# Performance work log

Measured on AMD Instinct MI355X. Metric: run time of the kernel, lower is better.

## Reference

```python
import jax, jax.numpy as jnp
import numpy as np

B, S, T = 32, 64, 64
E, H = 512, 512
V_SRC = 32000
V_TGT = 32000


def setup_inputs() -> dict:
    key = jax.random.key(0)
    ks = jax.random.split(key, 16)
    g = lambda i, shape: jax.random.normal(ks[i], shape, jnp.float32) * 0.05
    return {
        "src_sentences": jax.random.randint(ks[0], (B, S), 0, V_SRC),
        "target_sentences": jax.random.randint(ks[1], (B, T), 0, V_TGT),
        "source_sentence_length": jnp.full((B,), S, dtype=jnp.int32),
        "src_emb": g(2, (V_SRC, E)),
        "tgt_emb": g(3, (V_TGT, E)),
        "enc_Wih_f": g(4, (4 * H, E)), "enc_Whh_f": g(5, (4 * H, H)), "enc_b_f": jnp.zeros((4 * H,), jnp.float32),
        "enc_Wih_b": g(6, (4 * H, E)), "enc_Whh_b": g(7, (4 * H, H)), "enc_b_b": jnp.zeros((4 * H,), jnp.float32),
        "dec_Wih": g(8, (4 * H, E + H)), "dec_Whh": g(9, (4 * H, H)), "dec_b": jnp.zeros((4 * H,), jnp.float32),
        "W_att_src": g(10, (H, 2 * H)),
        "W_att_vec": g(11, (H, 3 * H)),
        "W_readout": g(12, (V_TGT, H)),
        "W_init": g(13, (H, 2 * H)), "b_init": jnp.zeros((H,), jnp.float32),
    }


def _lstm_cell(x, h, c, Wih, Whh, b):
    # PyTorch gate order: i, f, g, o ; b = b_ih + b_hh combined
    gates = x @ Wih.T + h @ Whh.T + b
    i, f, g, o = jnp.split(gates, 4, axis=-1)
    c_new = jax.nn.sigmoid(f) * c + jax.nn.sigmoid(i) * jnp.tanh(g)
    h_new = jax.nn.sigmoid(o) * jnp.tanh(c_new)
    return h_new, c_new


def _enc_dir(xs, lengths, Wih, Whh, b, reverse):
    # xs: [S, B, E]; emulates packed LSTM: state frozen / outputs zero at padded steps
    Sn, Bn, _ = xs.shape
    Hd = Whh.shape[1]
    ts = jnp.arange(Sn)

    def step(carry, inp):
        h, c = carry
        x, t = inp
        valid = (t < lengths)[:, None].astype(x.dtype)  # [B,1]
        h2, c2 = _lstm_cell(x, h, c, Wih, Whh, b)
        h = valid * h2 + (1.0 - valid) * h
        c = valid * c2 + (1.0 - valid) * c
        return (h, c), valid * h

    init = (jnp.zeros((Bn, Hd), xs.dtype), jnp.zeros((Bn, Hd), xs.dtype))
    (hT, cT), outs = jax.lax.scan(step, init, (xs, ts), reverse=reverse)
    return outs, hT, cT


def reference(src_sentences, target_sentences, source_sentence_length,
              src_emb, tgt_emb,
              enc_Wih_f, enc_Whh_f, enc_b_f,
              enc_Wih_b, enc_Whh_b, enc_b_b,
              dec_Wih, dec_Whh, dec_b,
              W_att_src, W_att_vec, W_readout, W_init, b_init):
    Bn, Sn = src_sentences.shape
    Hh = dec_Whh.shape[1]
    # faithful to original: embedding [B,S,E] then .view(S,B,E) (a reshape)
    src_x = src_emb[src_sentences].reshape(Sn, Bn, -1)  # [S,B,E]
    out_f, _, c_f = _enc_dir(src_x, source_sentence_length, enc_Wih_f, enc_Whh_f, enc_b_f, False)
    out_b, _, c_b = _enc_dir(src_x, source_sentence_length, enc_Wih_b, enc_Whh_b, enc_b_b, True)
    src_enc = jnp.concatenate([out_f, out_b], axis=-1).transpose(1, 0, 2)  # [B,S,2H]
    dec_c0 = jnp.concatenate([c_f, c_b], axis=-1) @ W_init.T + b_init
    dec_h0 = jnp.tanh(dec_c0)

    pad_mask = jnp.arange(Sn)[None, :] >= source_sentence_length[:, None]  # [B,S] True = pad
    src_att = src_enc @ W_att_src.T  # [B,S,H]
    ys = tgt_emb[target_sentences].transpose(1, 0, 2)  # [T,B,E]

    def dec_step(carry, y):
        h, c, att = carry
        x = jnp.concatenate([y, att], axis=-1)  # feed_input=True
        h, c = _lstm_cell(x, h, c, dec_Wih, dec_Whh, dec_b)
        score = jnp.einsum('bsh,bh->bs', src_att, h)
        score = jnp.where(pad_mask, -jnp.inf, score)
        alpha = jax.nn.softmax(score, axis=-1)
        ctx = jnp.einsum('bs,bsd->bd', alpha, src_enc)
        att = jnp.tanh(jnp.concatenate([h, ctx], axis=-1) @ W_att_vec.T)
        return (h, c, att), att

    att0 = jnp.zeros((Bn, Hh), src_x.dtype)
    _, att_ves = jax.lax.scan(dec_step, (dec_h0, dec_c0, att0), ys)  # [T,B,H]

    logp = jax.nn.log_softmax(att_ves @ W_readout.T, axis=-1)  # [T,B,V]
    logp = logp.transpose(1, 0, 2)  # [B,T,V]
    gold = jnp.take_along_axis(logp, target_sentences[:, :, None], axis=-1).squeeze(-1)  # [B,T]
    gold = gold * (target_sentences != 0).astype(logp.dtype)
    # faithful to original: permuted to batch-first then sum(dim=0) -> per-timestep sums, shape [T]
    return gold.sum(axis=0)
```

## Files before the change

kernel.cpp:

```cpp
#include <hip/hip_runtime.h>
#include <hip/hip_bf16.h>
#include <cmath>


__device__ __forceinline__ float sigf(float x){ return 1.0f/(1.0f+__expf(-x)); }

constexpr long o_senc   = 0;
constexpr long o_satt   = o_senc + 32L*64*1024;
constexpr long o_aves   = o_satt + 32L*64*512;
constexpr long o_hF     = o_aves + 64L*32*512;
constexpr long o_cF     = o_hF + 32L*512;
constexpr long o_hB     = o_cF + 32L*512;
constexpr long o_cB     = o_hB + 32L*512;
constexpr long o_sumexp = o_cB + 32L*512;
constexpr long o_gold   = o_sumexp + 2048;
constexpr long o_ccat   = o_gold + 2048;
constexpr long o_dech   = o_ccat + 32L*1024;
constexpr long o_decc   = o_dech + 32L*512;
constexpr long o_att    = o_decc + 32L*512;
constexpr long o_ctx    = o_att + 32L*512;
constexpr long o_gatesP = o_ctx + 32L*1024;
constexpr long o_attvP  = o_gatesP + 16L*65536;

__global__ void k_zero(float* p, int n){
    int i = blockIdx.x*256 + threadIdx.x;
    if (i < n) p[i] = 0.f;
}

__device__ __forceinline__ void gt_mac_store(const float (*Hs)[128], const float (*Ws)[129],
                                             float* __restrict__ P, int ldp, int n0){
    __syncthreads();
    int tid = threadIdx.x;
    int nl = tid & 63, bg = tid >> 6;
    float acc[8] = {};
    for (int k=0;k<128;++k){
        float w = Ws[nl][k];
        #pragma unroll
        for (int i=0;i<8;++i) acc[i] += Hs[bg*8+i][k] * w;
    }
    #pragma unroll
    for (int i=0;i<8;++i)
        P[(long)(bg*8+i)*ldp + n0 + nl] = acc[i];
}

__device__ __forceinline__ void gt_load_W(const float* __restrict__ W, int ldw, int kw, int n0,
                                          float (*Ws)[129]){
    int tid = threadIdx.x;
    int nl = tid >> 2, kl = (tid & 3) * 32;
    const float* wp = W + (long)(n0+nl)*ldw + kw + kl;
    #pragma unroll
    for (int i=0;i<32;i+=4){
        float4 v = *(const float4*)(wp + i);
        Ws[nl][kl+i+0]=v.x; Ws[nl][kl+i+1]=v.y; Ws[nl][kl+i+2]=v.z; Ws[nl][kl+i+3]=v.w;
    }
}

__device__ __forceinline__ void gates_tile_f32(
    const float* __restrict__ A, int lda, int k0,
    const float* __restrict__ W, int ldw, int kw, int n0,
    float* __restrict__ P, int ldp, float (*Hs)[128], float (*Ws)[129]){
    int tid = threadIdx.x;
    int bl = tid >> 3, kl = (tid & 7) * 16;
    const float* ap = A + (long)bl*lda + k0 + kl;
    float* hp = &Hs[bl][kl];
    #pragma unroll
    for (int i=0;i<16;i+=4){
        float4 v = *(const float4*)(ap + i);
        hp[i+0]=v.x; hp[i+1]=v.y; hp[i+2]=v.z; hp[i+3]=v.w;
    }
    gt_load_W(W, ldw, kw, n0, Ws);
    gt_mac_store(Hs, Ws, P, ldp, n0);
}

__device__ __forceinline__ void gates_tile_emb(
    const float* __restrict__ emb, const int* __restrict__ tok, int off, int stride, int k0,
    const float* __restrict__ W, int ldw, int kw, int n0,
    float* __restrict__ P, int ldp, float (*Hs)[128], float (*Ws)[129]){
    int tid = threadIdx.x;
    int bl = tid >> 3, kl = (tid & 7) * 16;
    const float* ap = emb + (long)tok[off + bl*stride]*512 + k0 + kl;
    float* hp = &Hs[bl][kl];
    #pragma unroll
    for (int i=0;i<16;i+=4){
        float4 v = *(const float4*)(ap + i);
        hp[i+0]=v.x; hp[i+1]=v.y; hp[i+2]=v.z; hp[i+3]=v.w;
    }
    gt_load_W(W, ldw, kw, n0, Ws);
    gt_mac_store(Hs, Ws, P, ldp, n0);
}

__global__ __launch_bounds__(256)
void k_enc_gates(const int* __restrict__ tok, const float* __restrict__ emb,
                 const float* __restrict__ hF, const float* __restrict__ hB,
                 const float* __restrict__ WihF, const float* __restrict__ WhhF,
                 const float* __restrict__ WihB, const float* __restrict__ WhhB,
                 float* __restrict__ gatesP, int s){
    __shared__ float Hs[32][128];
    __shared__ float Ws[64][129];
    int bx = blockIdx.x;
    int dir = bx >> 8, rem = bx & 255;
    int kc = rem & 7, nc = rem >> 3;
    int sd = dir ? 63 - s : s;
    float* P = gatesP + (long)(dir*8 + kc)*65536;
    if (kc < 4)
        gates_tile_emb(emb, tok, sd*32, 1, kc*128,
                       dir ? WihB : WihF, 512, kc*128, nc*64, P, 2048, Hs, Ws);
    else
        gates_tile_f32(dir ? hB : hF, 512, (kc-4)*128,
                       dir ? WhhB : WhhF, 512, (kc-4)*128, nc*64, P, 2048, Hs, Ws);
}

__global__ void k_enc_cell(const float* __restrict__ gatesP,
                           const float* __restrict__ bF, const float* __restrict__ bB,
                           float* hF, float* cF, float* hB, float* cB,
                           float* __restrict__ senc, const int* __restrict__ lens, int s){
    int idx = blockIdx.x*256 + threadIdx.x;
    int dir = idx >> 14, r = idx & 16383;
    int b = r >> 9, j = r & 511;
    int sd = dir ? (63 - s) : s;
    const float* P = gatesP + (long)dir*8*65536;
    const float* bias = dir ? bB : bF;
    float g[4];
    #pragma unroll
    for (int gi=0; gi<4; ++gi){
        int n = j + gi*512;
        float v = bias[n];
        #pragma unroll
        for (int kc=0; kc<8; ++kc) v += P[(long)kc*65536 + b*2048 + n];
        g[gi] = v;
    }
    float* hPtr = dir ? hB : hF;
    float* cPtr = dir ? cB : cF;
    float ho = hPtr[b*512+j], co = cPtr[b*512+j];
    float cn = sigf(g[1])*co + sigf(g[0])*tanhf(g[2]);
    float hn = sigf(g[3])*tanhf(cn);
    bool valid = sd < lens[b];
    hPtr[b*512+j] = valid ? hn : ho;
    cPtr[b*512+j] = valid ? cn : co;
    senc[(long)(b*64+sd)*1024 + dir*512 + j] = valid ? hn : 0.f;
}

__global__ void k_ccat(const float* __restrict__ cF, const float* __restrict__ cB,
                       float* __restrict__ ccat){
    int idx = blockIdx.x*256 + threadIdx.x;
    int b = idx >> 10, d = idx & 1023;
    ccat[idx] = (d < 512) ? cF[b*512+d] : cB[b*512+d-512];
}

__global__ __launch_bounds__(256)
void k_gemm(const float* __restrict__ A, const float* __restrict__ W,
            const float* __restrict__ bias, float* __restrict__ C,
            int M, int K, int lda, int ldw, int ldc){
    __shared__ float As[16][65];
    __shared__ float Wt[16][65];
    int tid = threadIdx.x;
    int m0 = blockIdx.x * 64, n0 = blockIdx.y * 64;
    int ty = tid >> 4, tx = tid & 15;
    int lm = tid >> 2, lk = (tid & 3) * 4;
    float acc[4][4] = {};
    for (int kt = 0; kt < K; kt += 16){
        float4 av;
        if (m0 + lm < M) av = *(const float4*)(A + (long)(m0+lm)*lda + kt + lk);
        else av = make_float4(0.f,0.f,0.f,0.f);
        As[lk+0][lm]=av.x; As[lk+1][lm]=av.y; As[lk+2][lm]=av.z; As[lk+3][lm]=av.w;
        float4 wv = *(const float4*)(W + (long)(n0+lm)*ldw + kt + lk);
        Wt[lk+0][lm]=wv.x; Wt[lk+1][lm]=wv.y; Wt[lk+2][lm]=wv.z; Wt[lk+3][lm]=wv.w;
        __syncthreads();
        #pragma unroll
        for (int k = 0; k < 16; ++k){
            float a0=As[k][ty*4+0], a1=As[k][ty*4+1], a2=As[k][ty*4+2], a3=As[k][ty*4+3];
            float b0=Wt[k][tx*4+0], b1=Wt[k][tx*4+1], b2=Wt[k][tx*4+2], b3=Wt[k][tx*4+3];
            acc[0][0]+=a0*b0; acc[0][1]+=a0*b1; acc[0][2]+=a0*b2; acc[0][3]+=a0*b3;
            acc[1][0]+=a1*b0; acc[1][1]+=a1*b1; acc[1][2]+=a1*b2; acc[1][3]+=a1*b3;
            acc[2][0]+=a2*b0; acc[2][1]+=a2*b1; acc[2][2]+=a2*b2; acc[2][3]+=a2*b3;
            acc[3][0]+=a3*b0; acc[3][1]+=a3*b1; acc[3][2]+=a3*b2; acc[3][3]+=a3*b3;
        }
        __syncthreads();
    }
    #pragma unroll
    for (int i=0;i<4;++i){
        int m = m0 + ty*4 + i;
        if (m >= M) continue;
        #pragma unroll
        for (int j=0;j<4;++j){
            int n = n0 + tx*4 + j;
            float v = acc[i][j];
            if (bias) v += bias[n];
            C[(long)m*ldc + n] = v;
        }
    }
}

__global__ void k_dec_init(const float* __restrict__ decc0, float* dech, float* att){
    int idx = blockIdx.x*256 + threadIdx.x;
    dech[idx] = tanhf(decc0[idx]);
    att[idx] = 0.f;
}

__global__ __launch_bounds__(256)
void k_dec_gates(const int* __restrict__ tok, const float* __restrict__ emb,
                 const float* __restrict__ att, const float* __restrict__ dech,
                 const float* __restrict__ Wih, const float* __restrict__ Whh,
                 float* __restrict__ gatesP, int t){
    __shared__ float Hs[32][128];
    __shared__ float Ws[64][129];
    int bx = blockIdx.x;
    int kc = bx % 12, nc = bx / 12;
    float* P = gatesP + (long)kc*65536;
    if (kc < 4)
        gates_tile_emb(emb, tok, t, 64, kc*128, Wih, 1024, kc*128, nc*64, P, 2048, Hs, Ws);
    else if (kc < 8)
        gates_tile_f32(att, 512, (kc-4)*128, Wih, 1024, 512 + (kc-4)*128, nc*64, P, 2048, Hs, Ws);
    else
        gates_tile_f32(dech, 512, (kc-8)*128, Whh, 512, (kc-8)*128, nc*64, P, 2048, Hs, Ws);
}

__global__ __launch_bounds__(256)
void k_dec_attn(const float* __restrict__ gatesP, const float* __restrict__ db,
                float* dech, float* decc,
                const float* __restrict__ satt, const float* __restrict__ senc,
                const int* __restrict__ lens, float* __restrict__ ctx){
    __shared__ float hS[512];
    __shared__ float scoreP[64][5];
    __shared__ float alphaS[64];
    int b = blockIdx.x, tid = threadIdx.x;
    #pragma unroll
    for (int jj=0; jj<2; ++jj){
        int j = tid + jj*256;
        float g[4];
        #pragma unroll
        for (int gi=0; gi<4; ++gi){
            int n = j + gi*512;
            float v = db[n];
            #pragma unroll
            for (int kc=0; kc<12; ++kc) v += gatesP[(long)kc*65536 + b*2048 + n];
            g[gi] = v;
        }
        float c = sigf(g[1])*decc[b*512+j] + sigf(g[0])*tanhf(g[2]);
        float h = sigf(g[3])*tanhf(c);
        decc[b*512+j] = c; dech[b*512+j] = h; hS[j] = h;
    }
    __syncthreads();
    {
        int si = tid >> 2, q = tid & 3;
        const float* sa = satt + (long)(b*64+si)*512 + q*128;
        float p = 0.f;
        for (int k=0;k<128;++k) p += sa[k]*hS[q*128+k];
        scoreP[si][q] = p;
    }
    __syncthreads();
    if (tid < 64){
        float sc = scoreP[tid][0]+scoreP[tid][1]+scoreP[tid][2]+scoreP[tid][3];
        if (tid >= lens[b]) sc = -INFINITY;
        float mx = sc;
        #pragma unroll
        for (int o=32;o>0;o>>=1) mx = fmaxf(mx, __shfl_xor(mx, o));
        float e = (sc == -INFINITY) ? 0.f : __expf(sc - mx);
        float sm = e;
        #pragma unroll
        for (int o=32;o>0;o>>=1) sm += __shfl_xor(sm, o);
        alphaS[tid] = e / fmaxf(sm, 1e-30f);
    }
    __syncthreads();
    float4 acc = make_float4(0.f,0.f,0.f,0.f);
    const float* sb = senc + (long)b*64*1024 + tid*4;
    for (int s2=0;s2<64;++s2){
        float a = alphaS[s2];
        float4 v = *(const float4*)(sb + s2*1024);
        acc.x += a*v.x; acc.y += a*v.y; acc.z += a*v.z; acc.w += a*v.w;
    }
    *(float4*)(ctx + b*1024 + tid*4) = acc;
}

__global__ __launch_bounds__(256)
void k_attvec(const float* __restrict__ dech, const float* __restrict__ ctx,
              const float* __restrict__ Wv, float* __restrict__ attvP){
    __shared__ float Hs[32][128];
    __shared__ float Ws[64][129];
    int bx = blockIdx.x;
    int kc = bx % 12, nc = bx / 12;
    float* P = attvP + (long)kc*16384;
    if (kc < 4)
        gates_tile_f32(dech, 512, kc*128, Wv, 1536, kc*128, nc*64, P, 512, Hs, Ws);
    else
        gates_tile_f32(ctx, 1024, (kc-4)*128, Wv, 1536, 512 + (kc-4)*128, nc*64, P, 512, Hs, Ws);
}

__global__ void k_attvec_fin(const float* __restrict__ attvP, float* att,
                             float* aves, int t){
    int idx = blockIdx.x*256 + threadIdx.x;
    int b = idx >> 9, j = idx & 511;
    float v = 0.f;
    #pragma unroll
    for (int kc=0; kc<12; ++kc) v += attvP[(long)kc*16384 + b*512 + j];
    v = tanhf(v);
    att[idx] = v;
    aves[(long)(t*32+b)*512 + j] = v;
}

__global__ __launch_bounds__(256)
void k_readout(const float* __restrict__ A, const float* __restrict__ W,
               float* __restrict__ sumexp){
    __shared__ float As[16][65];
    __shared__ float Wt[16][65];
    __shared__ float red[64][17];
    int tid = threadIdx.x;
    int m0 = blockIdx.x * 64, n0 = blockIdx.y * 64;
    int ty = tid >> 4, tx = tid & 15;
    int lm = tid >> 2, lk = (tid & 3) * 4;
    float acc[4][4] = {};
    for (int kt = 0; kt < 512; kt += 16){
        float4 av = *(const float4*)(A + (long)(m0+lm)*512 + kt + lk);
        As[lk+0][lm]=av.x; As[lk+1][lm]=av.y; As[lk+2][lm]=av.z; As[lk+3][lm]=av.w;
        float4 wv = *(const float4*)(W + (long)(n0+lm)*512 + kt + lk);
        Wt[lk+0][lm]=wv.x; Wt[lk+1][lm]=wv.y; Wt[lk+2][lm]=wv.z; Wt[lk+3][lm]=wv.w;
        __syncthreads();
        #pragma unroll
        for (int k = 0; k < 16; ++k){
            float a0=As[k][ty*4+0], a1=As[k][ty*4+1], a2=As[k][ty*4+2], a3=As[k][ty*4+3];
            float b0=Wt[k][tx*4+0], b1=Wt[k][tx*4+1], b2=Wt[k][tx*4+2], b3=Wt[k][tx*4+3];
            acc[0][0]+=a0*b0; acc[0][1]+=a0*b1; acc[0][2]+=a0*b2; acc[0][3]+=a0*b3;
            acc[1][0]+=a1*b0; acc[1][1]+=a1*b1; acc[1][2]+=a1*b2; acc[1][3]+=a1*b3;
            acc[2][0]+=a2*b0; acc[2][1]+=a2*b1; acc[2][2]+=a2*b2; acc[2][3]+=a2*b3;
            acc[3][0]+=a3*b0; acc[3][1]+=a3*b1; acc[3][2]+=a3*b2; acc[3][3]+=a3*b3;
        }
        __syncthreads();
    }
    #pragma unroll
    for (int i=0;i<4;++i){
        float rs = 0.f;
        #pragma unroll
        for (int j=0;j<4;++j) rs += __expf(acc[i][j]);
        red[ty*4+i][tx] = rs;
    }
    __syncthreads();
    if (tid < 64){
        float s = 0.f;
        #pragma unroll
        for (int x=0;x<16;++x) s += red[tid][x];
        atomicAdd(&sumexp[m0+tid], s);
    }
}

__global__ void k_gold(const float* __restrict__ aves, const float* __restrict__ Wr,
                       const int* __restrict__ tgt, float* __restrict__ gold){
    int wid = threadIdx.x >> 6, lane = threadIdx.x & 63;
    int m = blockIdx.x*4 + wid;
    int t = m >> 5, b = m & 31;
    int g = tgt[b*64 + t];
    const float* arow = aves + (long)m*512;
    const float* wrow = Wr + (long)g*512;
    float p = 0.f;
    for (int k=lane; k<512; k+=64) p += arow[k]*wrow[k];
    #pragma unroll
    for (int o=32;o>0;o>>=1) p += __shfl_xor(p, o);
    if (lane == 0) gold[m] = p;
}

__global__ void k_final(const float* __restrict__ gold, const float* __restrict__ sumexp,
                        const int* __restrict__ tgt, float* __restrict__ out){
    int t = threadIdx.x;
    float a = 0.f;
    for (int b=0;b<32;++b){
        int m = t*32 + b;
        float lp = gold[m] - logf(fmaxf(sumexp[m], 1e-30f));
        if (tgt[b*64 + t] != 0) a += lp;
    }
    out[t] = a;
}

extern "C" void kernel_launch(void* const* d_in, const int* in_sizes, int n_in,
                              void* d_out, int out_size, void* d_ws, size_t ws_size,
                              hipStream_t stream){
    const int* src_tok   = (const int*)d_in[0];
    const int* tgt_tok   = (const int*)d_in[1];
    const int* lens      = (const int*)d_in[2];
    const float* src_emb = (const float*)d_in[3];
    const float* tgt_emb = (const float*)d_in[4];
    const float* eWihF   = (const float*)d_in[5];
    const float* eWhhF   = (const float*)d_in[6];
    const float* ebF     = (const float*)d_in[7];
    const float* eWihB   = (const float*)d_in[8];
    const float* eWhhB   = (const float*)d_in[9];
    const float* ebB     = (const float*)d_in[10];
    const float* dWih    = (const float*)d_in[11];
    const float* dWhh    = (const float*)d_in[12];
    const float* db      = (const float*)d_in[13];
    const float* Wasrc   = (const float*)d_in[14];
    const float* Wavec   = (const float*)d_in[15];
    const float* Wread   = (const float*)d_in[16];
    const float* Winit   = (const float*)d_in[17];
    const float* binit   = (const float*)d_in[18];
    float* ws  = (float*)d_ws;
    float* out = (float*)d_out;

    float* senc = ws + o_senc;  float* satt = ws + o_satt; float* aves = ws + o_aves;
    float* hF = ws + o_hF; float* cF = ws + o_cF; float* hB = ws + o_hB; float* cB = ws + o_cB;
    float* sumexp = ws + o_sumexp; float* gold = ws + o_gold;
    float* ccat = ws + o_ccat;
    float* dech = ws + o_dech; float* decc = ws + o_decc; float* att = ws + o_att;
    float* ctx = ws + o_ctx;
    float* gatesP = ws + o_gatesP; float* attvP = ws + o_attvP;

    k_zero<<<264, 256, 0, stream>>>(hF, 67584);

    for (int s = 0; s < 64; ++s){
        k_enc_gates<<<512, 256, 0, stream>>>(src_tok, src_emb, hF, hB,
                                             eWihF, eWhhF, eWihB, eWhhB, gatesP, s);
        k_enc_cell<<<128, 256, 0, stream>>>(gatesP, ebF, ebB, hF, cF, hB, cB, senc, lens, s);
    }

    k_ccat<<<128, 256, 0, stream>>>(cF, cB, ccat);
    k_gemm<<<dim3(32,8), 256, 0, stream>>>(senc, Wasrc, nullptr, satt, 2048, 1024, 1024, 1024, 512);
    k_gemm<<<dim3(1,8), 256, 0, stream>>>(ccat, Winit, binit, decc, 32, 1024, 1024, 1024, 512);
    k_dec_init<<<64, 256, 0, stream>>>(decc, dech, att);

    for (int t = 0; t < 64; ++t){
        k_dec_gates<<<384, 256, 0, stream>>>(tgt_tok, tgt_emb, att, dech, dWih, dWhh, gatesP, t);
        k_dec_attn<<<32, 256, 0, stream>>>(gatesP, db, dech, decc, satt, senc, lens, ctx);
        k_attvec<<<96, 256, 0, stream>>>(dech, ctx, Wavec, attvP);
        k_attvec_fin<<<64, 256, 0, stream>>>(attvP, att, aves, t);
    }

    k_readout<<<dim3(32,500), 256, 0, stream>>>(aves, Wread, sumexp);
    k_gold<<<512, 256, 0, stream>>>(aves, Wread, tgt_tok, gold);
    k_final<<<1, 64, 0, stream>>>(gold, sumexp, tgt_tok, out);
}
```

Baseline: 4.779 ms.

## Hoist input projections into bf16 MFMA GEMMs and fuse attvec finalize into gates

```diff
diff --git a/kernel.cpp b/kernel.cpp
--- a/kernel.cpp
+++ b/kernel.cpp
@@ -4,6 +4,14 @@
 
 
 __device__ __forceinline__ float sigf(float x){ return 1.0f/(1.0f+__expf(-x)); }
+__device__ __forceinline__ short f2bf(float x){
+    unsigned u = __builtin_bit_cast(unsigned, x);
+    u += 0x7fff + ((u >> 16) & 1);
+    return (short)(u >> 16);
+}
+
+typedef __attribute__((ext_vector_type(8))) short short8;
+typedef __attribute__((ext_vector_type(4))) float float4v;
 
 constexpr long o_senc   = 0;
 constexpr long o_satt   = o_senc + 32L*64*1024;
@@ -22,9 +30,100 @@
 constexpr long o_gatesP = o_ctx + 32L*1024;
 constexpr long o_attvP  = o_gatesP + 16L*65536;
 
+__device__ __align__(16) float g_X[3][2048L*2048];
+__device__ __align__(16) short g_Wread_bf[32000L*512];
+__device__ __align__(16) short g_bfA[2][2048L*512];
+__device__ __align__(16) short g_bfW[3][2048L*512];
+__device__ __align__(16) short g_aves_bf[2048L*512];
+
 __global__ void k_zero(float* p, int n){
     int i = blockIdx.x*256 + threadIdx.x;
     if (i < n) p[i] = 0.f;
+}
+
+__global__ void k_cvt(const float* __restrict__ in, short* __restrict__ out, int ldin){
+    long idx = (long)blockIdx.x*256 + threadIdx.x;
+    long r = idx >> 9; int c = idx & 511;
+    out[idx] = f2bf(in[r*ldin + c]);
+}
+
+__global__ void k_gather_bf(const float* __restrict__ emb, const int* __restrict__ tok,
+                            short* __restrict__ out, int mode){
+    long idx = (long)blockIdx.x*256 + threadIdx.x;
+    int m = idx >> 9, e = idx & 511;
+    int ti = mode ? ((m & 31)*64 + (m >> 5)) : m;
+    out[idx] = f2bf(emb[(long)tok[ti]*512 + e]);
+}
+
+template<int STORE>
+__global__ __launch_bounds__(256)
+void k_mfma_gemm(const short* __restrict__ A, const short* __restrict__ B,
+                 float* __restrict__ C, int ldc){
+    __shared__ short As[128][72];
+    __shared__ short Bs[128][72];
+    int tid = threadIdx.x, l = tid & 63, w = tid >> 6;
+    int wm = w >> 1, wn = w & 1;
+    long m0 = (long)blockIdx.x * 128, n0 = (long)blockIdx.y * 128;
+    float4v acc[4][4];
+    #pragma unroll
+    for (int a=0;a<4;++a)
+        #pragma unroll
+        for (int b=0;b<4;++b)
+            #pragma unroll
+            for (int e=0;e<4;++e) acc[a][b][e] = 0.f;
+
+    for (int kb = 0; kb < 8; ++kb){
+        #pragma unroll
+        for (int i = tid; i < 1024; i += 256){
+            int r = i >> 3, c = i & 7;
+            *(uint4*)&As[r][c*8] = *(const uint4*)(A + (m0+r)*512 + kb*64 + c*8);
+            *(uint4*)&Bs[r][c*8] = *(const uint4*)(B + (n0+r)*512 + kb*64 + c*8);
+        }
+        __syncthreads();
+        #pragma unroll
+        for (int ks = 0; ks < 2; ++ks){
+            short8 af[4], bf[4];
+            #pragma unroll
+            for (int tm=0;tm<4;++tm)
+                af[tm] = *(const short8*)&As[wm*64 + tm*16 + (l&15)][ks*32 + (l>>4)*8];
+            #pragma unroll
+            for (int tn=0;tn<4;++tn)
+                bf[tn] = *(const short8*)&Bs[wn*64 + tn*16 + (l&15)][ks*32 + (l>>4)*8];
+            #pragma unroll
+            for (int tm=0;tm<4;++tm)
+                #pragma unroll
+                for (int tn=0;tn<4;++tn)
+                    acc[tm][tn] = __builtin_amdgcn_mfma_f32_16x16x32_bf16(
+                        af[tm], bf[tn], acc[tm][tn], 0, 0, 0);
+        }
+        __syncthreads();
+    }
+
+    int q = l >> 4;
+    if (STORE){
+        #pragma unroll
+        for (int tm=0;tm<4;++tm)
+            #pragma unroll
+            for (int r=0;r<4;++r){
+                long m = m0 + wm*64 + tm*16 + q*4 + r;
+                #pragma unroll
+                for (int tn=0;tn<4;++tn)
+                    C[m*ldc + n0 + wn*64 + tn*16 + (l&15)] = acc[tm][tn][r];
+            }
+    } else {
+        #pragma unroll
+        for (int tm=0;tm<4;++tm)
+            #pragma unroll
+            for (int r=0;r<4;++r){
+                float s = 0.f;
+                #pragma unroll
+                for (int tn=0;tn<4;++tn) s += __expf(acc[tm][tn][r]);
+                s += __shfl_xor(s, 1); s += __shfl_xor(s, 2);
+                s += __shfl_xor(s, 4); s += __shfl_xor(s, 8);
+                if ((l & 15) == 0)
+                    atomicAdd(&C[m0 + wm*64 + tm*16 + q*4 + r], s);
+            }
+    }
 }
 
 __device__ __forceinline__ void gt_mac_store(const float (*Hs)[128], const float (*Ws)[129],
@@ -72,42 +171,18 @@
     gt_mac_store(Hs, Ws, P, ldp, n0);
 }
 
-__device__ __forceinline__ void gates_tile_emb(
-    const float* __restrict__ emb, const int* __restrict__ tok, int off, int stride, int k0,
-    const float* __restrict__ W, int ldw, int kw, int n0,
-    float* __restrict__ P, int ldp, float (*Hs)[128], float (*Ws)[129]){
-    int tid = threadIdx.x;
-    int bl = tid >> 3, kl = (tid & 7) * 16;
-    const float* ap = emb + (long)tok[off + bl*stride]*512 + k0 + kl;
-    float* hp = &Hs[bl][kl];
-    #pragma unroll
-    for (int i=0;i<16;i+=4){
-        float4 v = *(const float4*)(ap + i);
-        hp[i+0]=v.x; hp[i+1]=v.y; hp[i+2]=v.z; hp[i+3]=v.w;
-    }
-    gt_load_W(W, ldw, kw, n0, Ws);
-    gt_mac_store(Hs, Ws, P, ldp, n0);
-}
-
 __global__ __launch_bounds__(256)
-void k_enc_gates(const int* __restrict__ tok, const float* __restrict__ emb,
-                 const float* __restrict__ hF, const float* __restrict__ hB,
-                 const float* __restrict__ WihF, const float* __restrict__ WhhF,
-                 const float* __restrict__ WihB, const float* __restrict__ WhhB,
-                 float* __restrict__ gatesP, int s){
+void k_enc_gates(const float* __restrict__ hF, const float* __restrict__ hB,
+                 const float* __restrict__ WhhF, const float* __restrict__ WhhB,
+                 float* __restrict__ gatesP){
     __shared__ float Hs[32][128];
     __shared__ float Ws[64][129];
     int bx = blockIdx.x;
-    int dir = bx >> 8, rem = bx & 255;
-    int kc = rem & 7, nc = rem >> 3;
-    int sd = dir ? 63 - s : s;
-    float* P = gatesP + (long)(dir*8 + kc)*65536;
-    if (kc < 4)
-        gates_tile_emb(emb, tok, sd*32, 1, kc*128,
-                       dir ? WihB : WihF, 512, kc*128, nc*64, P, 2048, Hs, Ws);
-    else
-        gates_tile_f32(dir ? hB : hF, 512, (kc-4)*128,
-                       dir ? WhhB : WhhF, 512, (kc-4)*128, nc*64, P, 2048, Hs, Ws);
+    int dir = bx >> 7, rem = bx & 127;
+    int kc = rem & 3, nc = rem >> 2;
+    float* P = gatesP + (long)(dir*4 + kc)*65536;
+    gates_tile_f32(dir ? hB : hF, 512, kc*128,
+                   dir ? WhhB : WhhF, 512, kc*128, nc*64, P, 2048, Hs, Ws);
 }
 
 __global__ void k_enc_cell(const float* __restrict__ gatesP,
@@ -118,15 +193,16 @@
     int dir = idx >> 14, r = idx & 16383;
     int b = r >> 9, j = r & 511;
     int sd = dir ? (63 - s) : s;
-    const float* P = gatesP + (long)dir*8*65536;
+    const float* P = gatesP + (long)dir*4*65536;
+    const float* X = g_X[dir];
     const float* bias = dir ? bB : bF;
     float g[4];
     #pragma unroll
     for (int gi=0; gi<4; ++gi){
         int n = j + gi*512;
-        float v = bias[n];
-        #pragma unroll
-        for (int kc=0; kc<8; ++kc) v += P[(long)kc*65536 + b*2048 + n];
+        float v = bias[n] + X[(long)(sd*32+b)*2048 + n];
+        #pragma unroll
+        for (int kc=0; kc<4; ++kc) v += P[(long)kc*65536 + b*2048 + n];
         g[gi] = v;
     }
     float* hPtr = dir ? hB : hF;
@@ -191,39 +267,64 @@
     }
 }
 
-__global__ void k_dec_init(const float* __restrict__ decc0, float* dech, float* att){
+__global__ void k_dec_init(const float* __restrict__ decc0, float* dech){
     int idx = blockIdx.x*256 + threadIdx.x;
     dech[idx] = tanhf(decc0[idx]);
-    att[idx] = 0.f;
 }
 
 __global__ __launch_bounds__(256)
-void k_dec_gates(const int* __restrict__ tok, const float* __restrict__ emb,
-                 const float* __restrict__ att, const float* __restrict__ dech,
+void k_dec_gates(const float* __restrict__ dech,
                  const float* __restrict__ Wih, const float* __restrict__ Whh,
-                 float* __restrict__ gatesP, int t){
+                 const float* __restrict__ attvP, float* __restrict__ gatesP,
+                 float* __restrict__ aves, int t){
     __shared__ float Hs[32][128];
     __shared__ float Ws[64][129];
-    int bx = blockIdx.x;
-    int kc = bx % 12, nc = bx / 12;
+    int bx = blockIdx.x, tid = threadIdx.x;
+    if (bx >= 256){
+        if (t == 0) return;
+        int idx = (bx-256)*256 + tid;
+        int b = idx >> 9, j = idx & 511;
+        float v = 0.f;
+        #pragma unroll
+        for (int kc=0; kc<12; ++kc) v += attvP[(long)kc*16384 + b*512 + j];
+        v = tanhf(v);
+        long m = (long)(t-1)*32 + b;
+        aves[m*512 + j] = v;
+        g_aves_bf[m*512 + j] = f2bf(v);
+        return;
+    }
+    int kc = bx & 7, nc = bx >> 3;
     float* P = gatesP + (long)kc*65536;
-    if (kc < 4)
-        gates_tile_emb(emb, tok, t, 64, kc*128, Wih, 1024, kc*128, nc*64, P, 2048, Hs, Ws);
-    else if (kc < 8)
-        gates_tile_f32(att, 512, (kc-4)*128, Wih, 1024, 512 + (kc-4)*128, nc*64, P, 2048, Hs, Ws);
-    else
-        gates_tile_f32(dech, 512, (kc-8)*128, Whh, 512, (kc-8)*128, nc*64, P, 2048, Hs, Ws);
+    if (kc < 4){
+        int bl = tid >> 3, kl = (tid & 7) * 16;
+        #pragma unroll
+        for (int i=0;i<16;++i){
+            float v = 0.f;
+            if (t > 0){
+                int col = kc*128 + kl + i;
+                #pragma unroll
+                for (int c12=0;c12<12;++c12) v += attvP[(long)c12*16384 + bl*512 + col];
+                v = tanhf(v);
+            }
+            Hs[bl][kl+i] = v;
+        }
+        gt_load_W(Wih, 1024, 512 + kc*128, nc*64, Ws);
+        gt_mac_store(Hs, Ws, P, 2048, nc*64);
+    } else {
+        gates_tile_f32(dech, 512, (kc-4)*128, Whh, 512, (kc-4)*128, nc*64, P, 2048, Hs, Ws);
+    }
 }
 
 __global__ __launch_bounds__(256)
 void k_dec_attn(const float* __restrict__ gatesP, const float* __restrict__ db,
                 float* dech, float* decc,
                 const float* __restrict__ satt, const float* __restrict__ senc,
-                const int* __restrict__ lens, float* __restrict__ ctx){
+                const int* __restrict__ lens, float* __restrict__ ctx, int t){
     __shared__ float hS[512];
     __shared__ float scoreP[64][5];
     __shared__ float alphaS[64];
     int b = blockIdx.x, tid = threadIdx.x;
+    const float* Yg = g_X[2];
     #pragma unroll
     for (int jj=0; jj<2; ++jj){
         int j = tid + jj*256;
@@ -231,9 +332,9 @@
         #pragma unroll
         for (int gi=0; gi<4; ++gi){
             int n = j + gi*512;
-            float v = db[n];
-            #pragma unroll
-            for (int kc=0; kc<12; ++kc) v += gatesP[(long)kc*65536 + b*2048 + n];
+            float v = db[n] + Yg[(long)(t*32+b)*2048 + n];
+            #pragma unroll
+            for (int kc=0; kc<8; ++kc) v += gatesP[(long)kc*65536 + b*2048 + n];
             g[gi] = v;
         }
         float c = sigf(g[1])*decc[b*512+j] + sigf(g[0])*tanhf(g[2]);
@@ -286,60 +387,16 @@
         gates_tile_f32(ctx, 1024, (kc-4)*128, Wv, 1536, 512 + (kc-4)*128, nc*64, P, 512, Hs, Ws);
 }
 
-__global__ void k_attvec_fin(const float* __restrict__ attvP, float* att,
-                             float* aves, int t){
+__global__ void k_aves_last(const float* __restrict__ attvP, float* __restrict__ aves){
     int idx = blockIdx.x*256 + threadIdx.x;
     int b = idx >> 9, j = idx & 511;
     float v = 0.f;
     #pragma unroll
     for (int kc=0; kc<12; ++kc) v += attvP[(long)kc*16384 + b*512 + j];
     v = tanhf(v);
-    att[idx] = v;
-    aves[(long)(t*32+b)*512 + j] = v;
-}
-
-__global__ __launch_bounds__(256)
-void k_readout(const float* __restrict__ A, const float* __restrict__ W,
-               float* __restrict__ sumexp){
-    __shared__ float As[16][65];
-    __shared__ float Wt[16][65];
-    __shared__ float red[64][17];
-    int tid = threadIdx.x;
-    int m0 = blockIdx.x * 64, n0 = blockIdx.y * 64;
-    int ty = tid >> 4, tx = tid & 15;
-    int lm = tid >> 2, lk = (tid & 3) * 4;
-    float acc[4][4] = {};
-    for (int kt = 0; kt < 512; kt += 16){
-        float4 av = *(const float4*)(A + (long)(m0+lm)*512 + kt + lk);
-        As[lk+0][lm]=av.x; As[lk+1][lm]=av.y; As[lk+2][lm]=av.z; As[lk+3][lm]=av.w;
-        float4 wv = *(const float4*)(W + (long)(n0+lm)*512 + kt + lk);
-        Wt[lk+0][lm]=wv.x; Wt[lk+1][lm]=wv.y; Wt[lk+2][lm]=wv.z; Wt[lk+3][lm]=wv.w;
-        __syncthreads();
-        #pragma unroll
-        for (int k = 0; k < 16; ++k){
-            float a0=As[k][ty*4+0], a1=As[k][ty*4+1], a2=As[k][ty*4+2], a3=As[k][ty*4+3];
-            float b0=Wt[k][tx*4+0], b1=Wt[k][tx*4+1], b2=Wt[k][tx*4+2], b3=Wt[k][tx*4+3];
-            acc[0][0]+=a0*b0; acc[0][1]+=a0*b1; acc[0][2]+=a0*b2; acc[0][3]+=a0*b3;
-            acc[1][0]+=a1*b0; acc[1][1]+=a1*b1; acc[1][2]+=a1*b2; acc[1][3]+=a1*b3;
-            acc[2][0]+=a2*b0; acc[2][1]+=a2*b1; acc[2][2]+=a2*b2; acc[2][3]+=a2*b3;
-            acc[3][0]+=a3*b0; acc[3][1]+=a3*b1; acc[3][2]+=a3*b2; acc[3][3]+=a3*b3;
-        }
-        __syncthreads();
-    }
-    #pragma unroll
-    for (int i=0;i<4;++i){
-        float rs = 0.f;
-        #pragma unroll
-        for (int j=0;j<4;++j) rs += __expf(acc[i][j]);
-        red[ty*4+i][tx] = rs;
-    }
-    __syncthreads();
-    if (tid < 64){
-        float s = 0.f;
-        #pragma unroll
-        for (int x=0;x<16;++x) s += red[tid][x];
-        atomicAdd(&sumexp[m0+tid], s);
-    }
+    long m = 63L*32 + b;
+    aves[m*512 + j] = v;
+    g_aves_bf[m*512 + j] = f2bf(v);
 }
 
 __global__ void k_gold(const float* __restrict__ aves, const float* __restrict__ Wr,
@@ -398,31 +455,53 @@
     float* hF = ws + o_hF; float* cF = ws + o_cF; float* hB = ws + o_hB; float* cB = ws + o_cB;
     float* sumexp = ws + o_sumexp; float* gold = ws + o_gold;
     float* ccat = ws + o_ccat;
-    float* dech = ws + o_dech; float* decc = ws + o_decc; float* att = ws + o_att;
+    float* dech = ws + o_dech; float* decc = ws + o_decc;
     float* ctx = ws + o_ctx;
     float* gatesP = ws + o_gatesP; float* attvP = ws + o_attvP;
 
+    float* Xf; short *WreadBf, *srcxBf, *tgtyBf, *WihFbf, *WihBbf, *dWihYbf;
+    hipGetSymbolAddress((void**)&Xf, HIP_SYMBOL(g_X));
+    hipGetSymbolAddress((void**)&WreadBf, HIP_SYMBOL(g_Wread_bf));
+    hipGetSymbolAddress((void**)&srcxBf, HIP_SYMBOL(g_bfA));
+    hipGetSymbolAddress((void**)&WihFbf, HIP_SYMBOL(g_bfW));
+    tgtyBf = srcxBf + 2048L*512;
+    WihBbf = WihFbf + 2048L*512;
+    dWihYbf = WihFbf + 2L*2048*512;
+    float* Xb = Xf + 2048L*2048;
+    float* Yg = Xf + 2L*2048*2048;
+
     k_zero<<<264, 256, 0, stream>>>(hF, 67584);
 
+    k_cvt<<<4096, 256, 0, stream>>>(eWihF, WihFbf, 512);
+    k_cvt<<<4096, 256, 0, stream>>>(eWihB, WihBbf, 512);
+    k_cvt<<<4096, 256, 0, stream>>>(dWih, dWihYbf, 1024);
+    k_cvt<<<64000, 256, 0, stream>>>(Wread, WreadBf, 512);
+    k_gather_bf<<<4096, 256, 0, stream>>>(src_emb, src_tok, srcxBf, 0);
+    k_gather_bf<<<4096, 256, 0, stream>>>(tgt_emb, tgt_tok, tgtyBf, 1);
+
+    k_mfma_gemm<1><<<dim3(16,16), 256, 0, stream>>>(srcxBf, WihFbf, Xf, 2048);
+    k_mfma_gemm<1><<<dim3(16,16), 256, 0, stream>>>(srcxBf, WihBbf, Xb, 2048);
+    k_mfma_gemm<1><<<dim3(16,16), 256, 0, stream>>>(tgtyBf, dWihYbf, Yg, 2048);
+
     for (int s = 0; s < 64; ++s){
-        k_enc_gates<<<512, 256, 0, stream>>>(src_tok, src_emb, hF, hB,
-                                             eWihF, eWhhF, eWihB, eWhhB, gatesP, s);
+        k_enc_gates<<<256, 256, 0, stream>>>(hF, hB, eWhhF, eWhhB, gatesP);
         k_enc_cell<<<128, 256, 0, stream>>>(gatesP, ebF, ebB, hF, cF, hB, cB, senc, lens, s);
     }
 
     k_ccat<<<128, 256, 0, stream>>>(cF, cB, ccat);
     k_gemm<<<dim3(32,8), 256, 0, stream>>>(senc, Wasrc, nullptr, satt, 2048, 1024, 1024, 1024, 512);
     k_gemm<<<dim3(1,8), 256, 0, stream>>>(ccat, Winit, binit, decc, 32, 1024, 1024, 1024, 512);
-    k_dec_init<<<64, 256, 0, stream>>>(decc, dech, att);
+    k_dec_init<<<64, 256, 0, stream>>>(decc, dech);
 
     for (int t = 0; t < 64; ++t){
-        k_dec_gates<<<384, 256, 0, stream>>>(tgt_tok, tgt_emb, att, dech, dWih, dWhh, gatesP, t);
-        k_dec_attn<<<32, 256, 0, stream>>>(gatesP, db, dech, decc, satt, senc, lens, ctx);
+        k_dec_gates<<<320, 256, 0, stream>>>(dech, dWih, dWhh, attvP, gatesP, aves, t);
+        k_dec_attn<<<32, 256, 0, stream>>>(gatesP, db, dech, decc, satt, senc, lens, ctx, t);
         k_attvec<<<96, 256, 0, stream>>>(dech, ctx, Wavec, attvP);
-        k_attvec_fin<<<64, 256, 0, stream>>>(attvP, att, aves, t);
-    }
-
-    k_readout<<<dim3(32,500), 256, 0, stream>>>(aves, Wread, sumexp);
+    }
+    k_aves_last<<<64, 256, 0, stream>>>(attvP, aves);
+
+    short* avesBf; hipGetSymbolAddress((void**)&avesBf, HIP_SYMBOL(g_aves_bf));
+    k_mfma_gemm<0><<<dim3(16,250), 256, 0, stream>>>(avesBf, WreadBf, sumexp, 0);
     k_gold<<<512, 256, 0, stream>>>(aves, Wread, tgt_tok, gold);
     k_final<<<1, 64, 0, stream>>>(gold, sumexp, tgt_tok, out);
 }
```

Measured after the change: 4.559 ms. -4.6%, faster.
